# Kernel optimization log

Measured on AMD Instinct MI355X. Metric: run time of the kernel, lower is better.

## Reference

```python
import jax, jax.numpy as jnp
import numpy as np

B, S, D, F, E = 4, 1024, 768, 3072, 8


def setup_inputs() -> dict:
    key = jax.random.key(0)
    k0, k1, k2, k3 = jax.random.split(key, 4)
    hidden_states = jax.random.normal(k0, (B, S, D), dtype=jnp.float32)
    w_router = jax.random.normal(k1, (D, E), dtype=jnp.float32) * 0.02
    w1 = jax.random.normal(k2, (E, D, F), dtype=jnp.float32) * 0.02
    b1 = jnp.zeros((E, F), dtype=jnp.float32)
    w2 = jax.random.normal(k3, (E, F, D), dtype=jnp.float32) * 0.02
    b2 = jnp.zeros((E, D), dtype=jnp.float32)
    return {"hidden_states": hidden_states, "w_router": w_router,
            "w1": w1, "b1": b1, "w2": w2, "b2": b2}


def reference(hidden_states, w_router, w1, b1, w2, b2):
    # Switch-style top-1 router: logits -> softmax -> one-hot mask + max prob
    router_logits = jnp.einsum("bsd,de->bse", hidden_states, w_router)
    router_probs_full = jax.nn.softmax(router_logits, axis=-1)
    expert_index = jnp.argmax(router_probs_full, axis=-1)            # [B,S] int
    router_probs = jnp.max(router_probs_full, axis=-1, keepdims=True)  # [B,S,1]
    router_mask = jax.nn.one_hot(expert_index, E, dtype=hidden_states.dtype)  # [B,S,E]

    # Dispatch/compute/combine: each token goes to exactly one expert FFN.
    # Loop over the small fixed expert set (E=8), combine via the one-hot mask;
    # math is identical to the gather -> expert FFN -> scatter of the original.
    out = jnp.zeros_like(hidden_states)
    for e in range(E):
        h = jax.nn.relu(jnp.einsum("bsd,df->bsf", hidden_states, w1[e]) + b1[e])
        h = jnp.einsum("bsf,fd->bsd", h, w2[e]) + b2[e]
        out = out + router_mask[..., e:e + 1] * h

    hidden_out = router_probs * out  # scale by top-1 router prob, as in original
    return hidden_out, router_logits, expert_index
```

## Files before the change

kernel.cpp:

```cpp
#include <hip/hip_runtime.h>
#include <hip/hip_bf16.h>

#define T_TOK 4096
#define DIM   768
#define FF    3072
#define NE    8
#define MAXTILES 48

typedef __attribute__((ext_vector_type(8))) short bf16x8;
typedef __attribute__((ext_vector_type(4))) short bf16x4;
typedef __attribute__((ext_vector_type(4))) float f32x4;
typedef __attribute__((ext_vector_type(2))) float f32x2;

typedef __attribute__((address_space(1))) void gvoid_t;
typedef __attribute__((address_space(3))) void lvoid_t;

__device__ __forceinline__ void g2l16(const void* g, void* l) {
    __builtin_amdgcn_global_load_lds((gvoid_t*)(void*)g, (lvoid_t*)l, 16, 0, 0);
}

#define WAIT_VM0() __builtin_amdgcn_s_waitcnt(0x0F70)
#define WAIT_VM4() __builtin_amdgcn_s_waitcnt(0x0F74)
#define WAIT_VM6() __builtin_amdgcn_s_waitcnt(0x0F76)
#define RAW_BARRIER() asm volatile("s_barrier" ::: "memory")

__device__ __forceinline__ unsigned short f2bf(float f) {
    union { float f; unsigned int u; } v; v.f = f;
    unsigned int u = v.u;
    u += 0x7FFFu + ((u >> 16) & 1u);
    return (unsigned short)(u >> 16);
}

__device__ __forceinline__ bf16x8 pack8(f32x4 a, f32x4 b) {
    bf16x8 r;
    r[0] = (short)f2bf(a[0]); r[1] = (short)f2bf(a[1]);
    r[2] = (short)f2bf(a[2]); r[3] = (short)f2bf(a[3]);
    r[4] = (short)f2bf(b[0]); r[5] = (short)f2bf(b[1]);
    r[6] = (short)f2bf(b[2]); r[7] = (short)f2bf(b[3]);
    return r;
}

__global__ __launch_bounds__(256) void k_router(
    const float* __restrict__ x, const float* __restrict__ wr,
    float* __restrict__ out_logits, float* __restrict__ out_eidx,
    float* __restrict__ probs, int* __restrict__ eidx_i,
    int* __restrict__ counts, int* __restrict__ bucket)
{
    int tok  = (blockIdx.x * 256 + threadIdx.x) >> 6;
    int lane = threadIdx.x & 63;
    if (tok >= T_TOK) return;
    const float* xr = x + (size_t)tok * DIM;
    float acc[NE];
    #pragma unroll
    for (int e = 0; e < NE; e++) acc[e] = 0.f;
    #pragma unroll
    for (int j = 0; j < DIM / 64; j++) {
        int d = j * 64 + lane;
        float xv = xr[d];
        const float* wrow = wr + (size_t)d * NE;
        #pragma unroll
        for (int e = 0; e < NE; e++) acc[e] += xv * wrow[e];
    }
    #pragma unroll
    for (int e = 0; e < NE; e++) {
        #pragma unroll
        for (int off = 32; off >= 1; off >>= 1)
            acc[e] += __shfl_xor(acc[e], off);
    }
    if (lane == 0) {
        float mx = acc[0]; int mi = 0;
        #pragma unroll
        for (int e = 1; e < NE; e++) if (acc[e] > mx) { mx = acc[e]; mi = e; }
        float se = 0.f;
        #pragma unroll
        for (int e = 0; e < NE; e++) se += __expf(acc[e] - mx);
        #pragma unroll
        for (int e = 0; e < NE; e++) out_logits[(size_t)tok * NE + e] = acc[e];
        out_eidx[tok] = (float)mi;
        eidx_i[tok] = mi;
        probs[tok] = 1.f / se;
        int pos = atomicAdd(&counts[mi], 1);
        bucket[mi * T_TOK + pos] = tok;
    }
}

__global__ void k_compact(const int* __restrict__ counts, int* __restrict__ offsets,
                          int* __restrict__ bucket, int* __restrict__ sorted)
{
    __shared__ int soff[NE + 1];
    if (threadIdx.x == 0) {
        int s = 0;
        for (int e = 0; e < NE; e++) { soff[e] = s; s += counts[e]; }
        soff[NE] = s;
        for (int e = 0; e <= NE; e++) offsets[e] = soff[e];
    }
    __syncthreads();
    for (int e = 0; e < NE; e++) {
        int c = counts[e], o = soff[e];
        for (int i = threadIdx.x; i < c; i += blockDim.x)
            sorted[o + i] = bucket[e * T_TOK + i];
    }
    __syncthreads();
    if (threadIdx.x == 0) {
        int nt = 0;
        for (int e = 0; e < NE; e++) {
            int c = counts[e];
            for (int t = 0; t * 128 < c && nt < MAXTILES; t++)
                bucket[nt++] = (e << 8) | t;
        }
        for (int i = nt; i < MAXTILES; i++) bucket[i] = -1;
    }
}

__global__ __launch_bounds__(256) void k_xconv(
    const float* __restrict__ x, unsigned short* __restrict__ Xb)
{
    int g0 = (blockIdx.x * 256 + threadIdx.x) * 8;
    if (g0 >= T_TOK * DIM) return;
    f32x4 a = *(const f32x4*)(x + g0);
    f32x4 b = *(const f32x4*)(x + g0 + 4);
    *(bf16x8*)(Xb + g0) = pack8(a, b);
}

__global__ __launch_bounds__(256) void k_tconv(
    const float* __restrict__ in, unsigned short* __restrict__ out, int R, int C)
{
    const size_t es = (size_t)R * C;
    in  += blockIdx.z * es;
    out += blockIdx.z * es;
    const int c0 = blockIdx.x * 64, r0 = blockIdx.y * 64;
    __shared__ unsigned short t[64][72];
    const int tr = threadIdx.x >> 2, tc = (threadIdx.x & 3) * 16;
    const float* src = in + (size_t)(r0 + tr) * C + c0 + tc;
    f32x4 v0 = *(const f32x4*)(src);
    f32x4 v1 = *(const f32x4*)(src + 4);
    f32x4 v2 = *(const f32x4*)(src + 8);
    f32x4 v3 = *(const f32x4*)(src + 12);
    const int xb = (tc >> 4) & 3;
    const int pr = (((tr >> 3) ^ xb) & 7) * 8 + (tr & 7);
    #pragma unroll
    for (int j = 0; j < 4; j++) {
        t[tc + j][pr]      = f2bf(v0[j]);
        t[tc + 4 + j][pr]  = f2bf(v1[j]);
        t[tc + 8 + j][pr]  = f2bf(v2[j]);
        t[tc + 12 + j][pr] = f2bf(v3[j]);
    }
    __syncthreads();
    const int oc = threadIdx.x >> 2, orr = (threadIdx.x & 3) * 16;
    const int rx = (oc >> 4) & 3;
    const int p0 = ((((orr >> 3) + 0) ^ rx) & 7) * 8;
    const int p1 = ((((orr >> 3) + 1) ^ rx) & 7) * 8;
    bf16x8 o0 = *(const bf16x8*)&t[oc][p0];
    bf16x8 o1 = *(const bf16x8*)&t[oc][p1];
    unsigned short* dst = out + (size_t)(c0 + oc) * R + r0 + orr;
    *(bf16x8*)(dst)     = o0;
    *(bf16x8*)(dst + 8) = o1;
}

__global__ __launch_bounds__(256, 2) void k_gemm1(
    const unsigned short* __restrict__ Xb, const unsigned short* __restrict__ wt1,
    const float* __restrict__ b1, const int* __restrict__ sorted,
    const int* __restrict__ counts, const int* __restrict__ offsets,
    const int* __restrict__ tile_tab, unsigned short* __restrict__ Hbuf)
{
    const int tv = tile_tab[blockIdx.y];
    if (tv < 0) return;
    const int e  = tv >> 8;
    const int ti = tv & 255;
    const int cnt = counts[e];
    const int n0 = blockIdx.x * 256;
    const int off = offsets[e];
    const int rbase = ti * 128;
    const int tid = threadIdx.x, lane = tid & 63, wave = tid >> 6;
    const int wm = wave >> 1, wn = wave & 1;

    __shared__ unsigned short As[3][128][32];
    __shared__ unsigned short Bs[3][256][32];

    const int lr = lane >> 2;
    const int ls = (lane & 3) * 8;

    int r0 = rbase + wave * 32 + lr;        if (r0 >= cnt) r0 = rbase;
    int r1 = rbase + wave * 32 + 16 + lr;   if (r1 >= cnt) r1 = rbase;
    const unsigned short* aP0 = Xb + (size_t)sorted[off + r0] * DIM + ls;
    const unsigned short* aP1 = Xb + (size_t)sorted[off + r1] * DIM + ls;
    const unsigned short* wB  = wt1 + (size_t)e * FF * DIM;
    const unsigned short* bP0 = wB + (size_t)(n0 + wave * 64 +  0 + lr) * DIM + ls;
    const unsigned short* bP1 = wB + (size_t)(n0 + wave * 64 + 16 + lr) * DIM + ls;
    const unsigned short* bP2 = wB + (size_t)(n0 + wave * 64 + 32 + lr) * DIM + ls;
    const unsigned short* bP3 = wB + (size_t)(n0 + wave * 64 + 48 + lr) * DIM + ls;

    f32x4 acc[4][8];
    #pragma unroll
    for (int i = 0; i < 4; i++)
        #pragma unroll
        for (int j = 0; j < 8; j++) acc[i][j] = (f32x4)0.f;

    const int lrow = lane & 15, kq = lane >> 4;
    const int NIT = DIM / 32;

#define STAGE1(bufi, ko) do { \
    g2l16(aP0 + (ko), &As[bufi][wave * 32][0]);       \
    g2l16(aP1 + (ko), &As[bufi][wave * 32 + 16][0]);  \
    g2l16(bP0 + (ko), &Bs[bufi][wave * 64][0]);       \
    g2l16(bP1 + (ko), &Bs[bufi][wave * 64 + 16][0]);  \
    g2l16(bP2 + (ko), &Bs[bufi][wave * 64 + 32][0]);  \
    g2l16(bP3 + (ko), &Bs[bufi][wave * 64 + 48][0]);  \
} while (0)

    STAGE1(0, 0);
    __syncthreads();
    STAGE1(1, 32);

    for (int it = 0; it < NIT; ++it) {
        const int buf = it % 3;
        if (it > 0) {
            if (it + 1 < NIT) WAIT_VM6(); else WAIT_VM0();
            RAW_BARRIER();
        }
        if (it + 2 < NIT) {
            STAGE1((it + 2) % 3, (it + 2) * 32);
        }
        bf16x8 af[4], bfv[8];
        #pragma unroll
        for (int i = 0; i < 4; i++)
            af[i] = *(const bf16x8*)&As[buf][wm * 64 + i * 16 + lrow][kq * 8];
        #pragma unroll
        for (int j = 0; j < 8; j++)
            bfv[j] = *(const bf16x8*)&Bs[buf][wn * 128 + j * 16 + lrow][kq * 8];
        #pragma unroll
        for (int mi = 0; mi < 4; mi++)
            #pragma unroll
            for (int ni = 0; ni < 8; ni++)
                acc[mi][ni] = __builtin_amdgcn_mfma_f32_16x16x32_bf16(
                    af[mi], bfv[ni], acc[mi][ni], 0, 0, 0);
    }
#undef STAGE1

    const int quad = lane >> 4;
    #pragma unroll
    for (int ni = 0; ni < 8; ni++) {
        int gn = n0 + wn * 128 + ni * 16 + lrow;
        float bias = b1[e * FF + gn];
        #pragma unroll
        for (int mi = 0; mi < 4; mi++) {
            f32x4 v = acc[mi][ni];
            #pragma unroll
            for (int r = 0; r < 4; r++) {
                int ml = rbase + wm * 64 + mi * 16 + quad * 4 + r;
                if (ml < cnt) {
                    float h = v[r] + bias; h = h > 0.f ? h : 0.f;
                    Hbuf[(size_t)(off + ml) * FF + gn] = f2bf(h);
                }
            }
        }
    }
}

__global__ __launch_bounds__(256, 3) void k_gemm2(
    const unsigned short* __restrict__ Hbuf, const unsigned short* __restrict__ wt2,
    const float* __restrict__ b2, const int* __restrict__ sorted,
    const int* __restrict__ counts, const int* __restrict__ offsets,
    const int* __restrict__ tile_tab, const float* __restrict__ probs,
    float* __restrict__ outh)
{
    const int tv = tile_tab[blockIdx.y];
    if (tv < 0) return;
    const int e  = tv >> 8;
    const int ti = tv & 255;
    const int cnt = counts[e];
    const int n0 = blockIdx.x * 128;
    const int kc = blockIdx.z;
    const int off = offsets[e];
    const int rbase = ti * 128;
    const int tid = threadIdx.x, lane = tid & 63, wave = tid >> 6;
    const int wm = wave >> 1, wn = wave & 1;

    __shared__ unsigned short As[3][128][32];
    __shared__ unsigned short Bs[3][128][32];
    __shared__ int   s_tok[128];
    __shared__ float s_prob[128];

    if (tid < 128) {
        int rr = rbase + tid; if (rr >= cnt) rr = rbase;
        int tk = sorted[off + rr];
        s_tok[tid]  = tk;
        s_prob[tid] = probs[tk];
    }

    const int lr = lane >> 2, ls = (lane & 3) * 8;
    int r0 = rbase + wave * 32 + lr;        if (r0 >= cnt) r0 = rbase;
    int r1 = rbase + wave * 32 + 16 + lr;   if (r1 >= cnt) r1 = rbase;
    const unsigned short* aP0 = Hbuf + (size_t)(off + r0) * FF + kc * 1024 + ls;
    const unsigned short* aP1 = Hbuf + (size_t)(off + r1) * FF + kc * 1024 + ls;
    const unsigned short* wB  = wt2 + (size_t)e * DIM * FF;
    const unsigned short* bP0 = wB + (size_t)(n0 + wave * 32 + lr) * FF + kc * 1024 + ls;
    const unsigned short* bP1 = wB + (size_t)(n0 + wave * 32 + 16 + lr) * FF + kc * 1024 + ls;

    f32x4 acc[4][4];
    #pragma unroll
    for (int i = 0; i < 4; i++)
        #pragma unroll
        for (int j = 0; j < 4; j++) acc[i][j] = (f32x4)0.f;

    const int lrow = lane & 15, kq = lane >> 4;
    const int NIT = 1024 / 32;

#define STAGE2(bufi, ko) do { \
    g2l16(aP0 + (ko), &As[bufi][wave * 32][0]);       \
    g2l16(aP1 + (ko), &As[bufi][wave * 32 + 16][0]);  \
    g2l16(bP0 + (ko), &Bs[bufi][wave * 32][0]);       \
    g2l16(bP1 + (ko), &Bs[bufi][wave * 32 + 16][0]);  \
} while (0)

    STAGE2(0, 0);
    __syncthreads();
    STAGE2(1, 32);

    for (int it = 0; it < NIT; ++it) {
        const int buf = it % 3;
        if (it > 0) {
            if (it + 1 < NIT) WAIT_VM4(); else WAIT_VM0();
            RAW_BARRIER();
        }
        if (it + 2 < NIT) {
            STAGE2((it + 2) % 3, (it + 2) * 32);
        }
        bf16x8 af[4], bfv[4];
        #pragma unroll
        for (int i = 0; i < 4; i++)
            af[i] = *(const bf16x8*)&As[buf][wm * 64 + i * 16 + lrow][kq * 8];
        #pragma unroll
        for (int i = 0; i < 4; i++)
            bfv[i] = *(const bf16x8*)&Bs[buf][wn * 64 + i * 16 + lrow][kq * 8];
        #pragma unroll
        for (int mi = 0; mi < 4; mi++)
            #pragma unroll
            for (int ni = 0; ni < 4; ni++)
                acc[mi][ni] = __builtin_amdgcn_mfma_f32_16x16x32_bf16(
                    af[mi], bfv[ni], acc[mi][ni], 0, 0, 0);
    }
#undef STAGE2

    const int quad = lane >> 4;
    #pragma unroll
    for (int ni = 0; ni < 4; ni++) {
        int gn = n0 + wn * 64 + ni * 16 + lrow;
        float bias = (kc == 0) ? b2[e * DIM + gn] : 0.f;
        #pragma unroll
        for (int mi = 0; mi < 4; mi++) {
            f32x4 v = acc[mi][ni];
            #pragma unroll
            for (int r = 0; r < 4; r++) {
                int mloc = wm * 64 + mi * 16 + quad * 4 + r;
                if (rbase + mloc < cnt) {
                    atomicAdd(&outh[(size_t)s_tok[mloc] * DIM + gn],
                              (v[r] + bias) * s_prob[mloc]);
                }
            }
        }
    }
}

__global__ __launch_bounds__(256) void k_gather_fb(
    const float* __restrict__ x, const int* __restrict__ sorted,
    unsigned short* __restrict__ Xg)
{
    int g0 = (blockIdx.x * 256 + threadIdx.x) * 8;
    if (g0 >= T_TOK * DIM) return;
    int row = g0 / DIM, col = g0 - row * DIM;
    const float* src = x + (size_t)sorted[row] * DIM + col;
    f32x4 a = *(const f32x4*)(src);
    f32x4 b = *(const f32x4*)(src + 4);
    *(bf16x8*)(Xg + (size_t)row * DIM + col) = pack8(a, b);
}

__global__ __launch_bounds__(256, 3) void k_gemm1_fb(
    const unsigned short* __restrict__ Xg, const float* __restrict__ w1,
    const float* __restrict__ b1, const int* __restrict__ counts,
    const int* __restrict__ offsets, unsigned short* __restrict__ Hbuf)
{
    const int e   = blockIdx.y >> 5;
    const int ti  = blockIdx.y & 31;
    const int cnt = counts[e];
    if (ti * 128 >= cnt) return;
    const int n0    = blockIdx.x * 128;
    const int off   = offsets[e];
    const int rbase = ti * 128;
    const int rmax  = cnt - rbase - 1;
    const int tid   = threadIdx.x;
    const int lane  = tid & 63;
    const int wave  = tid >> 6;
    const int wm = wave >> 1, wn = wave & 1;
    __shared__ unsigned short As[128][72];
    __shared__ unsigned short Bs[128][72];
    const float* w1e = w1 + (size_t)e * DIM * FF;
    f32x4 acc[4][4];
    #pragma unroll
    for (int i = 0; i < 4; i++)
        #pragma unroll
        for (int j = 0; j < 4; j++) acc[i][j] = (f32x4)0.f;
    const int arow = tid >> 1, aseg = tid & 1;
    const int are  = (arow <= rmax) ? arow : 0;
    const unsigned short* abase = Xg + (size_t)(off + rbase + are) * DIM + aseg * 32;
    const int kb = tid >> 5, nb = tid & 31;
    const float* bbase = w1e + (size_t)kb * 8 * FF + n0 + nb * 4;
    bf16x8 aR[4];
    f32x4  bR[8];
    #pragma unroll
    for (int j = 0; j < 4; j++) aR[j] = *(const bf16x8*)(abase + j * 8);
    #pragma unroll
    for (int r = 0; r < 8; r++) bR[r] = *(const f32x4*)(bbase + (size_t)r * FF);
    const int lrow = lane & 15, kq = lane >> 4;
    for (int it = 0; it < DIM / 64; ++it) {
        __syncthreads();
        #pragma unroll
        for (int j = 0; j < 4; j++)
            *(bf16x8*)&As[arow][aseg * 32 + j * 8] = aR[j];
        #pragma unroll
        for (int j = 0; j < 4; j++) {
            bf16x8 c;
            #pragma unroll
            for (int r = 0; r < 8; r++) c[r] = (short)f2bf(bR[r][j]);
            *(bf16x8*)&Bs[nb * 4 + j][kb * 8] = c;
        }
        __syncthreads();
        if (it + 1 < DIM / 64) {
            const unsigned short* an = abase + (it + 1) * 64;
            #pragma unroll
            for (int j = 0; j < 4; j++) aR[j] = *(const bf16x8*)(an + j * 8);
            const float* bn = bbase + (size_t)(it + 1) * 64 * FF;
            #pragma unroll
            for (int r = 0; r < 8; r++) bR[r] = *(const f32x4*)(bn + (size_t)r * FF);
        }
        #pragma unroll
        for (int ks = 0; ks < 2; ks++) {
            bf16x8 af[4], bfr[4];
            #pragma unroll
            for (int i = 0; i < 4; i++)
                af[i] = *(const bf16x8*)&As[wm * 64 + i * 16 + lrow][ks * 32 + kq * 8];
            #pragma unroll
            for (int i = 0; i < 4; i++)
                bfr[i] = *(const bf16x8*)&Bs[wn * 64 + i * 16 + lrow][ks * 32 + kq * 8];
            #pragma unroll
            for (int mi = 0; mi < 4; mi++)
                #pragma unroll
                for (int ni = 0; ni < 4; ni++)
                    acc[mi][ni] = __builtin_amdgcn_mfma_f32_16x16x32_bf16(
                        af[mi], bfr[ni], acc[mi][ni], 0, 0, 0);
        }
    }
    const int quad = lane >> 4;
    #pragma unroll
    for (int ni = 0; ni < 4; ni++) {
        int gn = n0 + wn * 64 + ni * 16 + lrow;
        float bias = b1[e * FF + gn];
        #pragma unroll
        for (int mi = 0; mi < 4; mi++) {
            f32x4 v = acc[mi][ni];
            #pragma unroll
            for (int r = 0; r < 4; r++) {
                int ml = wm * 64 + mi * 16 + quad * 4 + r;
                if (rbase + ml < cnt) {
                    float h = v[r] + bias;
                    h = h > 0.f ? h : 0.f;
                    Hbuf[(size_t)(off + rbase + ml) * FF + gn] = f2bf(h);
                }
            }
        }
    }
}

__global__ __launch_bounds__(256, 4) void k_gemm2_fb(
    const unsigned short* __restrict__ Hbuf, const float* __restrict__ w2,
    const float* __restrict__ b2, const int* __restrict__ sorted,
    const int* __restrict__ counts, const int* __restrict__ offsets,
    const float* __restrict__ probs, float* __restrict__ outh)
{
    const int e   = blockIdx.y >> 5;
    const int ti  = blockIdx.y & 31;
    const int cnt = counts[e];
    if (ti * 128 >= cnt) return;
    const int n0    = blockIdx.x * 64;
    const int off   = offsets[e];
    const int rbase = ti * 128;
    const int rmax  = cnt - rbase - 1;
    const int tid   = threadIdx.x;
    const int lane  = tid & 63;
    const int wave  = tid >> 6;
    const int wm = wave >> 1, wn = wave & 1;
    __shared__ unsigned short As[128][72];
    __shared__ unsigned short Bs[64][72];
    __shared__ int   s_tok[128];
    __shared__ float s_prob[128];
    if (tid < 128) {
        int r = rbase + tid;
        int tk = sorted[off + ((r < cnt) ? r : rbase)];
        s_tok[tid]  = tk;
        s_prob[tid] = probs[tk];
    }
    const float* w2e = w2 + (size_t)e * FF * DIM;
    f32x4 acc[4][2];
    #pragma unroll
    for (int i = 0; i < 4; i++)
        #pragma unroll
        for (int j = 0; j < 2; j++) acc[i][j] = (f32x4)0.f;
    const int arow = tid >> 1, aseg = tid & 1;
    const int are  = (arow <= rmax) ? arow : 0;
    const unsigned short* abase = Hbuf + (size_t)(off + rbase + are) * FF + aseg * 32;
    const int kb = tid >> 5, nb = tid & 31;
    const float* bbase = w2e + (size_t)kb * 8 * DIM + n0 + nb * 2;
    bf16x8 aR[4];
    f32x2  bR[8];
    #pragma unroll
    for (int j = 0; j < 4; j++) aR[j] = *(const bf16x8*)(abase + j * 8);
    #pragma unroll
    for (int r = 0; r < 8; r++) bR[r] = *(const f32x2*)(bbase + (size_t)r * DIM);
    const int lrow = lane & 15, kq = lane >> 4;
    for (int it = 0; it < FF / 64; ++it) {
        __syncthreads();
        #pragma unroll
        for (int j = 0; j < 4; j++)
            *(bf16x8*)&As[arow][aseg * 32 + j * 8] = aR[j];
        {
            bf16x8 c0, c1;
            #pragma unroll
            for (int r = 0; r < 8; r++) { c0[r] = (short)f2bf(bR[r][0]); c1[r] = (short)f2bf(bR[r][1]); }
            *(bf16x8*)&Bs[nb * 2 + 0][kb * 8] = c0;
            *(bf16x8*)&Bs[nb * 2 + 1][kb * 8] = c1;
        }
        __syncthreads();
        if (it + 1 < FF / 64) {
            const unsigned short* an = abase + (it + 1) * 64;
            #pragma unroll
            for (int j = 0; j < 4; j++) aR[j] = *(const bf16x8*)(an + j * 8);
            const float* bn = bbase + (size_t)(it + 1) * 64 * DIM;
            #pragma unroll
            for (int r = 0; r < 8; r++) bR[r] = *(const f32x2*)(bn + (size_t)r * DIM);
        }
        #pragma unroll
        for (int ks = 0; ks < 2; ks++) {
            bf16x8 af[4], bfr[2];
            #pragma unroll
            for (int i = 0; i < 4; i++)
                af[i] = *(const bf16x8*)&As[wm * 64 + i * 16 + lrow][ks * 32 + kq * 8];
            #pragma unroll
            for (int i = 0; i < 2; i++)
                bfr[i] = *(const bf16x8*)&Bs[wn * 32 + i * 16 + lrow][ks * 32 + kq * 8];
            #pragma unroll
            for (int mi = 0; mi < 4; mi++)
                #pragma unroll
                for (int ni = 0; ni < 2; ni++)
                    acc[mi][ni] = __builtin_amdgcn_mfma_f32_16x16x32_bf16(
                        af[mi], bfr[ni], acc[mi][ni], 0, 0, 0);
        }
    }
    const int quad = lane >> 4;
    #pragma unroll
    for (int ni = 0; ni < 2; ni++) {
        int gn = n0 + wn * 32 + ni * 16 + lrow;
        float bias = b2[e * DIM + gn];
        #pragma unroll
        for (int mi = 0; mi < 4; mi++) {
            f32x4 v = acc[mi][ni];
            #pragma unroll
            for (int r = 0; r < 4; r++) {
                int ml = wm * 64 + mi * 16 + quad * 4 + r;
                if (rbase + ml < cnt) {
                    outh[(size_t)s_tok[ml] * DIM + gn] = (v[r] + bias) * s_prob[ml];
                }
            }
        }
    }
}

extern "C" void kernel_launch(void* const* d_in, const int* in_sizes, int n_in,
                              void* d_out, int out_size, void* d_ws, size_t ws_size,
                              hipStream_t stream) {
    (void)in_sizes; (void)n_in; (void)out_size;
    const float* x  = (const float*)d_in[0];
    const float* wr = (const float*)d_in[1];
    const float* w1 = (const float*)d_in[2];
    const float* b1 = (const float*)d_in[3];
    const float* w2 = (const float*)d_in[4];
    const float* b2 = (const float*)d_in[5];

    float* out_hidden = (float*)d_out;
    float* out_logits = out_hidden + (size_t)T_TOK * DIM;
    float* out_eidx   = out_logits + (size_t)T_TOK * NE;

    char* ws = (char*)d_ws;
    int*   counts  = (int*)(ws + 0);
    int*   offsets = (int*)(ws + 64);
    float* probs   = (float*)(ws + 128);
    int*   eidx_i  = (int*)(ws + 16512);
    int*   sorted  = (int*)(ws + 32896);
    int*   bucket  = (int*)(ws + 49280);
    int*   tile_tab = bucket;
    unsigned short* Xb   = (unsigned short*)(ws + 180352);
    unsigned short* Hbuf = (unsigned short*)(ws + 6471808);
    unsigned short* wt1  = (unsigned short*)(ws + 31637632);
    unsigned short* wt2  = (unsigned short*)(ws + 69386368);
    const size_t NEED = 107135104;

    hipMemsetAsync(counts, 0, 32, stream);
    k_router<<<dim3(T_TOK / 4), dim3(256), 0, stream>>>(
        x, wr, out_logits, out_eidx, probs, eidx_i, counts, bucket);
    k_compact<<<dim3(1), dim3(256), 0, stream>>>(counts, offsets, bucket, sorted);

    if (ws_size >= NEED) {
        hipMemsetAsync(out_hidden, 0, (size_t)T_TOK * DIM * sizeof(float), stream);
        k_xconv<<<dim3(T_TOK * DIM / 8 / 256), dim3(256), 0, stream>>>(x, Xb);
        k_tconv<<<dim3(FF / 64, DIM / 64, NE), dim3(256), 0, stream>>>(w1, wt1, DIM, FF);
        k_tconv<<<dim3(DIM / 64, FF / 64, NE), dim3(256), 0, stream>>>(w2, wt2, FF, DIM);
        k_gemm1<<<dim3(FF / 256, MAXTILES), dim3(256), 0, stream>>>(
            Xb, wt1, b1, sorted, counts, offsets, tile_tab, Hbuf);
        k_gemm2<<<dim3(DIM / 128, MAXTILES, 3), dim3(256), 0, stream>>>(
            Hbuf, wt2, b2, sorted, counts, offsets, tile_tab, probs, out_hidden);
    } else {
        k_gather_fb<<<dim3(T_TOK * DIM / 8 / 256), dim3(256), 0, stream>>>(x, sorted, Xb);
        k_gemm1_fb<<<dim3(FF / 128, NE * 32), dim3(256), 0, stream>>>(
            Xb, w1, b1, counts, offsets, Hbuf);
        k_gemm2_fb<<<dim3(DIM / 64, NE * 32), dim3(256), 0, stream>>>(
            Hbuf, w2, b2, sorted, counts, offsets, probs, out_hidden);
    }
}
```

Measured before the change: 391.4 us.

## Fuse bf16 activation conversion into router and widen gemm2 tiles with XCD-aware mapping

The router kernel now writes the bf16 copy of the activations while it reads them, so the separate conversion kernel and its extra pass over x are removed. The down-projection GEMM tile grows from 128 to 256 output columns per block, which halves the grid and the re-reads of the H tile. Blocks are also remapped so neighbouring work lands on the same XCD. The wider tile doubles accumulator registers and LDS use, so the occupancy hint drops from 3 to 2. The fallback path still launches its gather kernel, which overwrites Xb after the router.

After: 391.6 us. No clear change (+0.1%).

```diff
diff --git a/kernel.cpp b/kernel.cpp
--- a/kernel.cpp
+++ b/kernel.cpp
@@ -44,12 +44,14 @@
     const float* __restrict__ x, const float* __restrict__ wr,
     float* __restrict__ out_logits, float* __restrict__ out_eidx,
     float* __restrict__ probs, int* __restrict__ eidx_i,
-    int* __restrict__ counts, int* __restrict__ bucket)
+    int* __restrict__ counts, int* __restrict__ bucket,
+    unsigned short* __restrict__ Xb)
 {
     int tok  = (blockIdx.x * 256 + threadIdx.x) >> 6;
     int lane = threadIdx.x & 63;
     if (tok >= T_TOK) return;
     const float* xr = x + (size_t)tok * DIM;
+    unsigned short* xbr = Xb + (size_t)tok * DIM;
     float acc[NE];
     #pragma unroll
     for (int e = 0; e < NE; e++) acc[e] = 0.f;
@@ -57,6 +59,7 @@
     for (int j = 0; j < DIM / 64; j++) {
         int d = j * 64 + lane;
         float xv = xr[d];
+        xbr[d] = f2bf(xv);
         const float* wrow = wr + (size_t)d * NE;
         #pragma unroll
         for (int e = 0; e < NE; e++) acc[e] += xv * wrow[e];
@@ -110,16 +113,6 @@
         }
         for (int i = nt; i < MAXTILES; i++) bucket[i] = -1;
     }
-}
-
-__global__ __launch_bounds__(256) void k_xconv(
-    const float* __restrict__ x, unsigned short* __restrict__ Xb)
-{
-    int g0 = (blockIdx.x * 256 + threadIdx.x) * 8;
-    if (g0 >= T_TOK * DIM) return;
-    f32x4 a = *(const f32x4*)(x + g0);
-    f32x4 b = *(const f32x4*)(x + g0 + 4);
-    *(bf16x8*)(Xb + g0) = pack8(a, b);
 }
 
 __global__ __launch_bounds__(256) void k_tconv(
@@ -257,27 +250,34 @@
     }
 }
 
-__global__ __launch_bounds__(256, 3) void k_gemm2(
+__global__ __launch_bounds__(256, 2) void k_gemm2(
     const unsigned short* __restrict__ Hbuf, const unsigned short* __restrict__ wt2,
     const float* __restrict__ b2, const int* __restrict__ sorted,
     const int* __restrict__ counts, const int* __restrict__ offsets,
     const int* __restrict__ tile_tab, const float* __restrict__ probs,
     float* __restrict__ outh)
 {
-    const int tv = tile_tab[blockIdx.y];
+    const int lid = blockIdx.x + 3 * (blockIdx.y + MAXTILES * blockIdx.z);
+    const int xcd = lid & 7;
+    const int j_  = lid >> 3;
+    const int m   = j_ % 3;
+    const int g   = (j_ / 3) * 8 + xcd;
+    const int by  = g % MAXTILES;
+    const int kc  = g / MAXTILES;
+
+    const int tv = tile_tab[by];
     if (tv < 0) return;
     const int e  = tv >> 8;
     const int ti = tv & 255;
     const int cnt = counts[e];
-    const int n0 = blockIdx.x * 128;
-    const int kc = blockIdx.z;
+    const int n0 = m * 256;
     const int off = offsets[e];
     const int rbase = ti * 128;
     const int tid = threadIdx.x, lane = tid & 63, wave = tid >> 6;
     const int wm = wave >> 1, wn = wave & 1;
 
     __shared__ unsigned short As[3][128][32];
-    __shared__ unsigned short Bs[3][128][32];
+    __shared__ unsigned short Bs[3][256][32];
     __shared__ int   s_tok[128];
     __shared__ float s_prob[128];
 
@@ -294,14 +294,16 @@
     const unsigned short* aP0 = Hbuf + (size_t)(off + r0) * FF + kc * 1024 + ls;
     const unsigned short* aP1 = Hbuf + (size_t)(off + r1) * FF + kc * 1024 + ls;
     const unsigned short* wB  = wt2 + (size_t)e * DIM * FF;
-    const unsigned short* bP0 = wB + (size_t)(n0 + wave * 32 + lr) * FF + kc * 1024 + ls;
-    const unsigned short* bP1 = wB + (size_t)(n0 + wave * 32 + 16 + lr) * FF + kc * 1024 + ls;
-
-    f32x4 acc[4][4];
+    const unsigned short* bP0 = wB + (size_t)(n0 + wave * 64 +  0 + lr) * FF + kc * 1024 + ls;
+    const unsigned short* bP1 = wB + (size_t)(n0 + wave * 64 + 16 + lr) * FF + kc * 1024 + ls;
+    const unsigned short* bP2 = wB + (size_t)(n0 + wave * 64 + 32 + lr) * FF + kc * 1024 + ls;
+    const unsigned short* bP3 = wB + (size_t)(n0 + wave * 64 + 48 + lr) * FF + kc * 1024 + ls;
+
+    f32x4 acc[4][8];
     #pragma unroll
     for (int i = 0; i < 4; i++)
         #pragma unroll
-        for (int j = 0; j < 4; j++) acc[i][j] = (f32x4)0.f;
+        for (int j = 0; j < 8; j++) acc[i][j] = (f32x4)0.f;
 
     const int lrow = lane & 15, kq = lane >> 4;
     const int NIT = 1024 / 32;
@@ -309,8 +311,10 @@
 #define STAGE2(bufi, ko) do { \
     g2l16(aP0 + (ko), &As[bufi][wave * 32][0]);       \
     g2l16(aP1 + (ko), &As[bufi][wave * 32 + 16][0]);  \
-    g2l16(bP0 + (ko), &Bs[bufi][wave * 32][0]);       \
-    g2l16(bP1 + (ko), &Bs[bufi][wave * 32 + 16][0]);  \
+    g2l16(bP0 + (ko), &Bs[bufi][wave * 64][0]);       \
+    g2l16(bP1 + (ko), &Bs[bufi][wave * 64 + 16][0]);  \
+    g2l16(bP2 + (ko), &Bs[bufi][wave * 64 + 32][0]);  \
+    g2l16(bP3 + (ko), &Bs[bufi][wave * 64 + 48][0]);  \
 } while (0)
 
     STAGE2(0, 0);
@@ -320,23 +324,23 @@
     for (int it = 0; it < NIT; ++it) {
         const int buf = it % 3;
         if (it > 0) {
-            if (it + 1 < NIT) WAIT_VM4(); else WAIT_VM0();
+            if (it + 1 < NIT) WAIT_VM6(); else WAIT_VM0();
             RAW_BARRIER();
         }
         if (it + 2 < NIT) {
             STAGE2((it + 2) % 3, (it + 2) * 32);
         }
-        bf16x8 af[4], bfv[4];
+        bf16x8 af[4], bfv[8];
         #pragma unroll
         for (int i = 0; i < 4; i++)
             af[i] = *(const bf16x8*)&As[buf][wm * 64 + i * 16 + lrow][kq * 8];
         #pragma unroll
-        for (int i = 0; i < 4; i++)
-            bfv[i] = *(const bf16x8*)&Bs[buf][wn * 64 + i * 16 + lrow][kq * 8];
+        for (int j = 0; j < 8; j++)
+            bfv[j] = *(const bf16x8*)&Bs[buf][wn * 128 + j * 16 + lrow][kq * 8];
         #pragma unroll
         for (int mi = 0; mi < 4; mi++)
             #pragma unroll
-            for (int ni = 0; ni < 4; ni++)
+            for (int ni = 0; ni < 8; ni++)
                 acc[mi][ni] = __builtin_amdgcn_mfma_f32_16x16x32_bf16(
                     af[mi], bfv[ni], acc[mi][ni], 0, 0, 0);
     }
@@ -344,8 +348,8 @@
 
     const int quad = lane >> 4;
     #pragma unroll
-    for (int ni = 0; ni < 4; ni++) {
-        int gn = n0 + wn * 64 + ni * 16 + lrow;
+    for (int ni = 0; ni < 8; ni++) {
+        int gn = n0 + wn * 128 + ni * 16 + lrow;
         float bias = (kc == 0) ? b2[e * DIM + gn] : 0.f;
         #pragma unroll
         for (int mi = 0; mi < 4; mi++) {
@@ -605,17 +609,16 @@
 
     hipMemsetAsync(counts, 0, 32, stream);
     k_router<<<dim3(T_TOK / 4), dim3(256), 0, stream>>>(
-        x, wr, out_logits, out_eidx, probs, eidx_i, counts, bucket);
+        x, wr, out_logits, out_eidx, probs, eidx_i, counts, bucket, Xb);
     k_compact<<<dim3(1), dim3(256), 0, stream>>>(counts, offsets, bucket, sorted);
 
     if (ws_size >= NEED) {
         hipMemsetAsync(out_hidden, 0, (size_t)T_TOK * DIM * sizeof(float), stream);
-        k_xconv<<<dim3(T_TOK * DIM / 8 / 256), dim3(256), 0, stream>>>(x, Xb);
         k_tconv<<<dim3(FF / 64, DIM / 64, NE), dim3(256), 0, stream>>>(w1, wt1, DIM, FF);
         k_tconv<<<dim3(DIM / 64, FF / 64, NE), dim3(256), 0, stream>>>(w2, wt2, FF, DIM);
         k_gemm1<<<dim3(FF / 256, MAXTILES), dim3(256), 0, stream>>>(
             Xb, wt1, b1, sorted, counts, offsets, tile_tab, Hbuf);
-        k_gemm2<<<dim3(DIM / 128, MAXTILES, 3), dim3(256), 0, stream>>>(
+        k_gemm2<<<dim3(DIM / 256, MAXTILES, 3), dim3(256), 0, stream>>>(
             Hbuf, wt2, b2, sorted, counts, offsets, tile_tab, probs, out_hidden);
     } else {
         k_gather_fb<<<dim3(T_TOK * DIM / 8 / 256), dim3(256), 0, stream>>>(x, sorted, Xb);
```

## Fuse x conversion and output zeroing into router, merge tconv launches, swizzle gemm2 grid

Applied to the files above, without the earlier changes.

The router kernel now also writes the bf16 copy of x and zeroes the output rows, which removes the separate xconv kernel and the output memset. The two weight-transpose launches become one launch with a z-split. The gemm2 block index is remapped so consecutive blocks land on the same XCD and share tile data. These steps cut launch overhead and improve L2 locality, but the router now does scalar 2-byte stores and the fallback path writes Xb redundantly before gather overwrites it.

After: 376.1 us. 3.9% less time.

```diff
diff --git a/kernel.cpp b/kernel.cpp
--- a/kernel.cpp
+++ b/kernel.cpp
@@ -44,12 +44,20 @@
     const float* __restrict__ x, const float* __restrict__ wr,
     float* __restrict__ out_logits, float* __restrict__ out_eidx,
     float* __restrict__ probs, int* __restrict__ eidx_i,
-    int* __restrict__ counts, int* __restrict__ bucket)
+    int* __restrict__ counts, int* __restrict__ bucket,
+    unsigned short* __restrict__ Xb, float* __restrict__ outh)
 {
     int tok  = (blockIdx.x * 256 + threadIdx.x) >> 6;
     int lane = threadIdx.x & 63;
     if (tok >= T_TOK) return;
+    {
+        float* o = outh + (size_t)tok * DIM;
+        #pragma unroll
+        for (int j = 0; j < DIM / 256; j++)
+            *(f32x4*)(o + j * 256 + lane * 4) = (f32x4)0.f;
+    }
     const float* xr = x + (size_t)tok * DIM;
+    unsigned short* xbr = Xb + (size_t)tok * DIM;
     float acc[NE];
     #pragma unroll
     for (int e = 0; e < NE; e++) acc[e] = 0.f;
@@ -57,6 +65,7 @@
     for (int j = 0; j < DIM / 64; j++) {
         int d = j * 64 + lane;
         float xv = xr[d];
+        xbr[d] = f2bf(xv);
         const float* wrow = wr + (size_t)d * NE;
         #pragma unroll
         for (int e = 0; e < NE; e++) acc[e] += xv * wrow[e];
@@ -112,23 +121,24 @@
     }
 }
 
-__global__ __launch_bounds__(256) void k_xconv(
-    const float* __restrict__ x, unsigned short* __restrict__ Xb)
-{
-    int g0 = (blockIdx.x * 256 + threadIdx.x) * 8;
-    if (g0 >= T_TOK * DIM) return;
-    f32x4 a = *(const f32x4*)(x + g0);
-    f32x4 b = *(const f32x4*)(x + g0 + 4);
-    *(bf16x8*)(Xb + g0) = pack8(a, b);
-}
-
 __global__ __launch_bounds__(256) void k_tconv(
-    const float* __restrict__ in, unsigned short* __restrict__ out, int R, int C)
-{
-    const size_t es = (size_t)R * C;
-    in  += blockIdx.z * es;
-    out += blockIdx.z * es;
-    const int c0 = blockIdx.x * 64, r0 = blockIdx.y * 64;
+    const float* __restrict__ w1, unsigned short* __restrict__ wt1,
+    const float* __restrict__ w2, unsigned short* __restrict__ wt2)
+{
+    int R, C, c0, r0;
+    const float* in;
+    unsigned short* out;
+    if (blockIdx.z < NE) {
+        R = DIM; C = FF;
+        in  = w1  + (size_t)blockIdx.z * R * C;
+        out = wt1 + (size_t)blockIdx.z * R * C;
+        c0 = blockIdx.x * 64; r0 = blockIdx.y * 64;
+    } else {
+        R = FF; C = DIM;
+        in  = w2  + (size_t)(blockIdx.z - NE) * R * C;
+        out = wt2 + (size_t)(blockIdx.z - NE) * R * C;
+        c0 = blockIdx.y * 64; r0 = blockIdx.x * 64;
+    }
     __shared__ unsigned short t[64][72];
     const int tr = threadIdx.x >> 2, tc = (threadIdx.x & 3) * 16;
     const float* src = in + (size_t)(r0 + tr) * C + c0 + tc;
@@ -264,13 +274,20 @@
     const int* __restrict__ tile_tab, const float* __restrict__ probs,
     float* __restrict__ outh)
 {
-    const int tv = tile_tab[blockIdx.y];
+    const int lid = blockIdx.x + 6 * blockIdx.y + 288 * blockIdx.z;
+    const int xcd = lid & 7;
+    const int j_  = lid >> 3;
+    const int m   = j_ % 6;
+    const int gg  = (j_ / 6) * 8 + xcd;
+    const int by  = gg % MAXTILES;
+    const int kc  = gg / MAXTILES;
+
+    const int tv = tile_tab[by];
     if (tv < 0) return;
     const int e  = tv >> 8;
     const int ti = tv & 255;
     const int cnt = counts[e];
-    const int n0 = blockIdx.x * 128;
-    const int kc = blockIdx.z;
+    const int n0 = m * 128;
     const int off = offsets[e];
     const int rbase = ti * 128;
     const int tid = threadIdx.x, lane = tid & 63, wave = tid >> 6;
@@ -604,20 +621,20 @@
     const size_t NEED = 107135104;
 
     hipMemsetAsync(counts, 0, 32, stream);
-    k_router<<<dim3(T_TOK / 4), dim3(256), 0, stream>>>(
-        x, wr, out_logits, out_eidx, probs, eidx_i, counts, bucket);
-    k_compact<<<dim3(1), dim3(256), 0, stream>>>(counts, offsets, bucket, sorted);
 
     if (ws_size >= NEED) {
-        hipMemsetAsync(out_hidden, 0, (size_t)T_TOK * DIM * sizeof(float), stream);
-        k_xconv<<<dim3(T_TOK * DIM / 8 / 256), dim3(256), 0, stream>>>(x, Xb);
-        k_tconv<<<dim3(FF / 64, DIM / 64, NE), dim3(256), 0, stream>>>(w1, wt1, DIM, FF);
-        k_tconv<<<dim3(DIM / 64, FF / 64, NE), dim3(256), 0, stream>>>(w2, wt2, FF, DIM);
+        k_router<<<dim3(T_TOK / 4), dim3(256), 0, stream>>>(
+            x, wr, out_logits, out_eidx, probs, eidx_i, counts, bucket, Xb, out_hidden);
+        k_compact<<<dim3(1), dim3(256), 0, stream>>>(counts, offsets, bucket, sorted);
+        k_tconv<<<dim3(48, 12, 2 * NE), dim3(256), 0, stream>>>(w1, wt1, w2, wt2);
         k_gemm1<<<dim3(FF / 256, MAXTILES), dim3(256), 0, stream>>>(
             Xb, wt1, b1, sorted, counts, offsets, tile_tab, Hbuf);
         k_gemm2<<<dim3(DIM / 128, MAXTILES, 3), dim3(256), 0, stream>>>(
             Hbuf, wt2, b2, sorted, counts, offsets, tile_tab, probs, out_hidden);
     } else {
+        k_router<<<dim3(T_TOK / 4), dim3(256), 0, stream>>>(
+            x, wr, out_logits, out_eidx, probs, eidx_i, counts, bucket, Xb, out_hidden);
+        k_compact<<<dim3(1), dim3(256), 0, stream>>>(counts, offsets, bucket, sorted);
         k_gather_fb<<<dim3(T_TOK * DIM / 8 / 256), dim3(256), 0, stream>>>(x, sorted, Xb);
         k_gemm1_fb<<<dim3(FF / 128, NE * 32), dim3(256), 0, stream>>>(
             Xb, w1, b1, counts, offsets, Hbuf);
```
